# Kernel optimization log

Measured on AMD Instinct MI355X. Metric: run time of the kernel, lower is better.

The kernel has to match this reference:

```python
import jax, jax.numpy as jnp
import numpy as np

EPS_BN = 1e-5
EPS_COS = 1e-8
N, E, D = 50000, 1600000, 128
HGC, LG, NUM_CLASSES, EIN, PAE_H = 64, 4, 2, 12, 128


def setup_inputs() -> dict:
    key = jax.random.key(0)
    ks = jax.random.split(key, 16)
    kaiming = lambda k, fi, fo: jax.random.normal(k, (fi, fo), jnp.float32) * (2.0 / fi) ** 0.5
    glorot = lambda k, shape: jax.random.normal(k, shape, jnp.float32) * (2.0 / (shape[-2] + shape[-1])) ** 0.5
    inp = {}
    inp["features"] = jax.random.normal(ks[0], (N, D), jnp.float32)
    inp["edge_index"] = jax.random.randint(ks[1], (2, E), 0, N, jnp.int32)
    inp["edgenet_input"] = jax.random.normal(ks[2], (E, EIN), jnp.float32)
    # PAE parser: Linear(6,128) -> ReLU -> BN(128) -> Dropout -> Linear(128,128)
    inp["pae_w1"] = kaiming(ks[3], EIN // 2, PAE_H)
    inp["pae_b1"] = jnp.zeros((PAE_H,), jnp.float32)
    inp["pae_bn_g"] = jnp.ones((PAE_H,), jnp.float32)
    inp["pae_bn_b"] = jnp.zeros((PAE_H,), jnp.float32)
    inp["pae_bn_rm"] = jnp.zeros((PAE_H,), jnp.float32)
    inp["pae_bn_rv"] = jnp.ones((PAE_H,), jnp.float32)
    inp["pae_w2"] = kaiming(ks[4], PAE_H, PAE_H)
    inp["pae_b2"] = jnp.zeros((PAE_H,), jnp.float32)
    # ChebConv weights, K=3, bias=False: [K, in, out]
    inp["cheb_w0"] = glorot(ks[5], (3, D, HGC))
    inp["cheb_w1"] = glorot(ks[6], (3, HGC, HGC))
    inp["cheb_w2"] = glorot(ks[7], (3, HGC, HGC))
    inp["cheb_w3"] = glorot(ks[8], (3, HGC, HGC))
    # classifier: Linear(lg*hgc=256, 256) -> ReLU -> BN(256) -> Linear(256, num_classes)
    CLS_IN = LG * HGC
    inp["cls_w1"] = kaiming(ks[9], CLS_IN, 256)
    inp["cls_b1"] = jnp.zeros((256,), jnp.float32)
    inp["cls_bn_g"] = jnp.ones((256,), jnp.float32)
    inp["cls_bn_b"] = jnp.zeros((256,), jnp.float32)
    inp["cls_bn_rm"] = jnp.zeros((256,), jnp.float32)
    inp["cls_bn_rv"] = jnp.ones((256,), jnp.float32)
    inp["cls_w2"] = kaiming(ks[10], 256, NUM_CLASSES)
    inp["cls_b2"] = jnp.zeros((NUM_CLASSES,), jnp.float32)
    return inp


def _bn_eval(h, g, b, rm, rv):
    return (h - rm) * jax.lax.rsqrt(rv + EPS_BN) * g + b


def _pae(x, w1, b1, g, b, rm, rv, w2, b2):
    half = w1.shape[0]
    def enc(z):
        h = jax.nn.relu(z @ w1 + b1)
        h = _bn_eval(h, g, b, rm, rv)
        return h @ w2 + b2                      # [E, PAE_H]
    h1, h2 = enc(x[:, :half]), enc(x[:, half:])
    num = jnp.sum(h1 * h2, axis=1)
    den = jnp.maximum(jnp.linalg.norm(h1, axis=1) * jnp.linalg.norm(h2, axis=1), EPS_COS)
    return (num / den + 1.0) * 0.5              # cosine sim mapped to [0, 1]


def _cheb_conv(x, W, row, col, norm, n_nodes):
    # (the +I from L and the -I self-loops with fill=-1 cancel in the propagation)
    def lhat(z):
        return jax.ops.segment_sum(norm[:, None] * z[col], row, num_segments=n_nodes)
    Tx0 = x
    Tx1 = lhat(Tx0)
    Tx2 = 2.0 * lhat(Tx1) - Tx0
    return Tx0 @ W[0] + Tx1 @ W[1] + Tx2 @ W[2]


def reference(features, edge_index, edgenet_input,
              pae_w1, pae_b1, pae_bn_g, pae_bn_b, pae_bn_rm, pae_bn_rv, pae_w2, pae_b2,
              cheb_w0, cheb_w1, cheb_w2, cheb_w3,
              cls_w1, cls_b1, cls_bn_g, cls_bn_b, cls_bn_rm, cls_bn_rv, cls_w2, cls_b2):
    n_nodes = features.shape[0]
    row, col = edge_index[0], edge_index[1]
    # learned edge weights
    edge_weight = _pae(edgenet_input, pae_w1, pae_b1, pae_bn_g, pae_bn_b,
                       pae_bn_rm, pae_bn_rv, pae_w2, pae_b2)
    # sym-normalized (negative) adjacency weights of the scaled Laplacian
    deg = jax.ops.segment_sum(edge_weight, row, num_segments=n_nodes)
    dis = jnp.where(deg > 0, jax.lax.rsqrt(jnp.where(deg > 0, deg, 1.0)), 0.0)
    norm = -dis[row] * edge_weight * dis[col]
    # GCN stack with jumping-knowledge concat (eval mode: dropout is identity)
    h = jax.nn.relu(_cheb_conv(features, cheb_w0, row, col, norm, n_nodes))
    jk = h
    for W in (cheb_w1, cheb_w2, cheb_w3):
        h = jax.nn.relu(_cheb_conv(h, W, row, col, norm, n_nodes))
        jk = jnp.concatenate((jk, h), axis=1)
    # classifier head
    z = jax.nn.relu(jk @ cls_w1 + cls_b1)
    z = _bn_eval(z, cls_bn_g, cls_bn_b, cls_bn_rm, cls_bn_rv)
    logit = z @ cls_w2 + cls_b2
    return (jk, logit, edge_weight)
```

## Files before the change

kernel.cpp:

```cpp
#include <hip/hip_runtime.h>

#define NN 50000
#define EE 1600000

using u16 = unsigned short;
using u32 = unsigned int;
using u64 = unsigned long long;

typedef float f32x4 __attribute__((ext_vector_type(4)));
typedef __bf16 bf16x8 __attribute__((ext_vector_type(8)));
typedef unsigned short u16x8 __attribute__((ext_vector_type(8)));

struct alignas(8) U16x4 { u16 a, b, c, d; };
struct PtrTab { const void* p[20]; };

#define OW1 0
#define OB1 768
#define OG 896
#define OBB 1024
#define ORM 1152
#define ORV 1280
#define OW2 1408
#define OB2 17792
#define OCH0 17920
#define OCH1 42496
#define OCH2 54784
#define OCH3 67072
#define OCW1 79360
#define OCB1 144896
#define OCG 145152
#define OCBB 145408
#define OCRM 145664
#define OCRV 145920
#define OCW2 146176
#define OCB2 146688
#define OTOT 146690

#define LG_OFF ((size_t)NN * 256)
#define EW_OFF ((size_t)NN * 256 + (size_t)NN * 2)

__device__ __forceinline__ float bf2f(u16 u) { return __builtin_bit_cast(float, (u32)u << 16); }
__device__ __forceinline__ float bfl(u32 u) { return __builtin_bit_cast(float, u << 16); }
__device__ __forceinline__ float bfh(u32 u) { return __builtin_bit_cast(float, u & 0xffff0000u); }
__device__ __forceinline__ u16 f2bf(float f) {
    u32 u = __builtin_bit_cast(u32, f);
    return (u16)((u + 0x7fffu + ((u >> 16) & 1u)) >> 16);
}

__global__ __launch_bounds__(256) void k_detect(const u16* __restrict__ f, int* __restrict__ flag) {
    __shared__ int bad;
    if (threadIdx.x == 0) bad = 0;
    __syncthreads();
    u16 u = f[threadIdx.x];
    int e = (u >> 7) & 0xFF;
    if (e >= 0x90) atomicAdd(&bad, 1);
    __syncthreads();
    if (threadIdx.x == 0) flag[0] = (bad < 16) ? 1 : 0;
}

__global__ __launch_bounds__(256) void k_wconv(PtrTab tab, const int* __restrict__ flag,
                                               float* __restrict__ wpad) {
    const int SZ[20] = {768, 128, 128, 128, 128, 128, 16384, 128, 24576, 12288, 12288, 12288,
                        65536, 256, 256, 256, 256, 256, 512, 2};
    const int OF[20] = {OW1, OB1, OG, OBB, ORM, ORV, OW2, OB2, OCH0, OCH1, OCH2, OCH3,
                        OCW1, OCB1, OCG, OCBB, OCRM, OCRV, OCW2, OCB2};
    int a = blockIdx.x;
    int n = SZ[a];
    float* dst = wpad + OF[a];
    if (flag[0] != 0) {
        const u16* s = (const u16*)tab.p[a];
        for (int i = threadIdx.x; i < n; i += 256) dst[i] = bf2f(s[i]);
    } else {
        const float* s = (const float*)tab.p[a];
        for (int i = threadIdx.x; i < n; i += 256) dst[i] = s[i];
    }
}

__global__ __launch_bounds__(128) void k_fold(const float* __restrict__ wpad,
                                              u16* __restrict__ W2s, float* __restrict__ b2p) {
    const float* g = wpad + OG;
    const float* b = wpad + OBB;
    const float* rm = wpad + ORM;
    const float* rv = wpad + ORV;
    const float* w2 = wpad + OW2;
    const float* b2 = wpad + OB2;
    int blk = blockIdx.x, tid = threadIdx.x;
    if (blk < 32) {
        int kc = blk >> 3, jt = blk & 7;
        int lane = tid & 63, jh = tid >> 6;
        int q = lane >> 4;
        for (int jj = 0; jj < 4; jj++) {
            int j = jh * 4 + jj;
            int k = kc * 32 + ((j < 4) ? (q * 4 + j) : (16 + q * 4 + (j - 4)));
            int jcol = jt * 16 + (lane & 15);
            float s = g[k] * rsqrtf(rv[k] + 1e-5f);
            W2s[((kc * 8 + jt) * 64 + lane) * 8 + j] = f2bf(s * w2[k * 128 + jcol]);
        }
    } else {
        if (tid < 128) {
            int j = tid;
            float acc = b2[j];
            for (int k = 0; k < 128; k++) {
                float s = g[k] * rsqrtf(rv[k] + 1e-5f);
                float t = b[k] - rm[k] * s;
                acc += t * w2[k * 128 + j];
            }
            b2p[j] = acc;
        }
    }
}

__global__ __launch_bounds__(256) void k_foldc(const float* __restrict__ wpad,
                                               u16* __restrict__ W1c, float* __restrict__ w2p,
                                               float* __restrict__ b2p2) {
    int tid = threadIdx.x;
    if (blockIdx.x < 64) {
        const float* w1 = wpad + OCW1;
        int base = blockIdx.x * 1024 + tid * 4;
#pragma unroll
        for (int u = 0; u < 4; u++) {
            int gi = base + u;
            int j = gi & 7;
            int lane = (gi >> 3) & 63;
            int ct = (gi >> 9) & 15;
            int kc2 = (gi >> 13) & 1;
            int l = gi >> 14;
            int k = l * 64 + kc2 * 32 + ((lane >> 4) & 3) * 8 + j;
            int col = ct * 16 + (lane & 15);
            W1c[gi] = f2bf(w1[k * 256 + col]);
        }
    } else {
        __shared__ float red[8];
        int j = tid;
        float s = wpad[OCG + j] * rsqrtf(wpad[OCRV + j] + 1e-5f);
        float t = wpad[OCBB + j] - wpad[OCRM + j] * s;
        float w0 = wpad[OCW2 + j * 2], w1v = wpad[OCW2 + j * 2 + 1];
        w2p[j * 2] = s * w0;
        w2p[j * 2 + 1] = s * w1v;
        float c0 = t * w0, c1 = t * w1v;
#pragma unroll
        for (int off = 1; off < 64; off <<= 1) {
            c0 += __shfl_xor(c0, off);
            c1 += __shfl_xor(c1, off);
        }
        int wv = tid >> 6, lane = tid & 63;
        if (lane == 0) { red[wv * 2] = c0; red[wv * 2 + 1] = c1; }
        __syncthreads();
        if (tid == 0) b2p2[0] = wpad[OCB2] + red[0] + red[2] + red[4] + red[6];
        if (tid == 1) b2p2[1] = wpad[OCB2 + 1] + red[1] + red[3] + red[5] + red[7];
    }
}

__global__ __launch_bounds__(256) void k_foldw(const float* __restrict__ wpad,
                                               u16* __restrict__ Wf0, u16* __restrict__ Wf1,
                                               u16* __restrict__ Wf2, u16* __restrict__ Wf3) {
    int b = blockIdx.x, tid = threadIdx.x;
    const float* src;
    u16* dst;
    int nkt;
    if (b < 24)      { src = wpad + OCH0; dst = Wf0; nkt = 12; }
    else if (b < 36) { src = wpad + OCH1; dst = Wf1; b -= 24; nkt = 6; }
    else if (b < 48) { src = wpad + OCH2; dst = Wf2; b -= 36; nkt = 6; }
    else             { src = wpad + OCH3; dst = Wf3; b -= 48; nkt = 6; }
    int base = b * 1024 + tid * 4;
#pragma unroll
    for (int u = 0; u < 4; u++) {
        int gi = base + u;
        int jj = gi & 7;
        int lane = (gi >> 3) & 63;
        int ct = (gi >> 9) & 3;
        int kt = gi >> 11;
        if (kt < nkt) {
            int k = kt * 32 + ((lane >> 4) & 3) * 8 + jj;
            int col = ct * 16 + (lane & 15);
            dst[gi] = f2bf(src[k * 64 + col]);
        }
    }
}

__global__ __launch_bounds__(256) void k_x0(const void* __restrict__ feat, const int* __restrict__ flag,
                                            u16* __restrict__ X0) {
    int i = blockIdx.x * 256 + threadIdx.x;
    if (flag[0] != 0) {
        ((uint4*)X0)[i] = ((const uint4*)feat)[i];
    } else {
        const float4* f = (const float4*)feat;
        float4 a = f[2 * i], b = f[2 * i + 1];
        u16x8 o;
        o[0] = f2bf(a.x); o[1] = f2bf(a.y); o[2] = f2bf(a.z); o[3] = f2bf(a.w);
        o[4] = f2bf(b.x); o[5] = f2bf(b.y); o[6] = f2bf(b.z); o[7] = f2bf(b.w);
        ((uint4*)X0)[i] = __builtin_bit_cast(uint4, o);
    }
}

__global__ __launch_bounds__(256, 3) void k_pae(const void* __restrict__ zin, const float* __restrict__ wpad,
                                                const u16* __restrict__ W2sg, const float* __restrict__ b2p,
                                                const int* __restrict__ ei, const int* __restrict__ flag,
                                                float* __restrict__ ewf, void* __restrict__ dout,
                                                u64* __restrict__ dc) {
    __shared__ __align__(16) u16 sW2[16384];
    __shared__ float sB2[128];
    int tid = threadIdx.x;
    for (int i = tid; i < 8192; i += 256) ((u32*)sW2)[i] = ((const u32*)W2sg)[i];
    if (tid < 128) sB2[tid] = b2p[tid];
    __syncthreads();

    bool isbf = flag[0] != 0;
    int wv = __builtin_amdgcn_readfirstlane(tid >> 6);
    int lane = tid & 63;
    int quad = lane >> 4, lrow = lane & 15, jc = lane & 15;
    u32 qm = (quad == 0) ? 0xffffffffu : 0u;

    uint4 w1f[8];
    f32x4 cb[8];
#pragma unroll
    for (int kt = 0; kt < 8; kt++) {
        u32 a = 0, b = 0, c = 0;
        if (quad == 0) {
            int col = kt * 16 + lrow;
            a = (u32)f2bf(wpad[OW1 + 0 * 128 + col]) | ((u32)f2bf(wpad[OW1 + 1 * 128 + col]) << 16);
            b = (u32)f2bf(wpad[OW1 + 2 * 128 + col]) | ((u32)f2bf(wpad[OW1 + 3 * 128 + col]) << 16);
            c = (u32)f2bf(wpad[OW1 + 4 * 128 + col]) | ((u32)f2bf(wpad[OW1 + 5 * 128 + col]) << 16);
        }
        w1f[kt] = (uint4){a, b, c, 0u};
#pragma unroll
        for (int r = 0; r < 4; r++) cb[kt][r] = wpad[OB1 + kt * 16 + quad * 4 + r];
    }

    int gw = blockIdx.x * 4 + wv;
    const int ngroups = EE / 16;
    const int gstep = gridDim.x * 4;

    uint2 pb0, pb1, pb2;
    float4 pf0, pf1, pf2;
    if (gw < ngroups) {
        if (isbf) {
            const uint2* zp = (const uint2*)((const u16*)zin + (size_t)(gw * 16 + lrow) * 12);
            pb0 = zp[0]; pb1 = zp[1]; pb2 = zp[2];
        } else {
            const float4* zp = (const float4*)((const float*)zin + (size_t)(gw * 16 + lrow) * 12);
            pf0 = zp[0]; pf1 = zp[1]; pf2 = zp[2];
        }
    }

#pragma unroll 1
    for (int gidx = gw; gidx < ngroups; gidx += gstep) {
        int e0 = gidx * 16;
        float z1[6], z2[6];
        if (isbf) {
            z1[0] = bfl(pb0.x); z1[1] = bfh(pb0.x); z1[2] = bfl(pb0.y); z1[3] = bfh(pb0.y);
            z1[4] = bfl(pb1.x); z1[5] = bfh(pb1.x);
            z2[0] = bfl(pb1.y); z2[1] = bfh(pb1.y); z2[2] = bfl(pb2.x); z2[3] = bfh(pb2.x);
            z2[4] = bfl(pb2.y); z2[5] = bfh(pb2.y);
        } else {
            z1[0] = pf0.x; z1[1] = pf0.y; z1[2] = pf0.z; z1[3] = pf0.w; z1[4] = pf1.x; z1[5] = pf1.y;
            z2[0] = pf1.z; z2[1] = pf1.w; z2[2] = pf2.x; z2[3] = pf2.y; z2[4] = pf2.z; z2[5] = pf2.w;
        }
        int gn = gidx + gstep;
        if (gn < ngroups) {
            if (isbf) {
                const uint2* zp = (const uint2*)((const u16*)zin + (size_t)(gn * 16 + lrow) * 12);
                pb0 = zp[0]; pb1 = zp[1]; pb2 = zp[2];
            } else {
                const float4* zp = (const float4*)((const float*)zin + (size_t)(gn * 16 + lrow) * 12);
                pf0 = zp[0]; pf1 = zp[1]; pf2 = zp[2];
            }
        }
        int rows[4];
        if (jc == 0) {
#pragma unroll
            for (int r = 0; r < 4; r++) rows[r] = ei[e0 + quad * 4 + r];
        }

        u32 za0, za1, za2, zb0, zb1, zb2;
        asm("v_cvt_pk_bf16_f32 %0, %1, %2" : "=v"(za0) : "v"(z1[0]), "v"(z1[1]));
        asm("v_cvt_pk_bf16_f32 %0, %1, %2" : "=v"(za1) : "v"(z1[2]), "v"(z1[3]));
        asm("v_cvt_pk_bf16_f32 %0, %1, %2" : "=v"(za2) : "v"(z1[4]), "v"(z1[5]));
        asm("v_cvt_pk_bf16_f32 %0, %1, %2" : "=v"(zb0) : "v"(z2[0]), "v"(z2[1]));
        asm("v_cvt_pk_bf16_f32 %0, %1, %2" : "=v"(zb1) : "v"(z2[2]), "v"(z2[3]));
        asm("v_cvt_pk_bf16_f32 %0, %1, %2" : "=v"(zb2) : "v"(z2[4]), "v"(z2[5]));
        uint4 zu1 = {za0 & qm, za1 & qm, za2 & qm, 0u};
        uint4 zu2 = {zb0 & qm, zb1 & qm, zb2 & qm, 0u};
        bf16x8 zf1 = __builtin_bit_cast(bf16x8, zu1);
        bf16x8 zf2 = __builtin_bit_cast(bf16x8, zu2);

        bf16x8 a1f[4], a2f[4];
        {
            f32x4 c1[8];
#pragma unroll
            for (int kt = 0; kt < 8; kt++)
                c1[kt] = __builtin_amdgcn_mfma_f32_16x16x32_bf16(
                    __builtin_bit_cast(bf16x8, w1f[kt]), zf1, cb[kt], 0, 0, 0);
#pragma unroll
            for (int kc = 0; kc < 4; kc++) {
                float h0 = fmaxf(c1[2 * kc][0], 0.f), h1 = fmaxf(c1[2 * kc][1], 0.f);
                float h2 = fmaxf(c1[2 * kc][2], 0.f), h3 = fmaxf(c1[2 * kc][3], 0.f);
                float h4 = fmaxf(c1[2 * kc + 1][0], 0.f), h5 = fmaxf(c1[2 * kc + 1][1], 0.f);
                float h6 = fmaxf(c1[2 * kc + 1][2], 0.f), h7 = fmaxf(c1[2 * kc + 1][3], 0.f);
                u32 p0, p1, p2, p3;
                asm("v_cvt_pk_bf16_f32 %0, %1, %2" : "=v"(p0) : "v"(h0), "v"(h1));
                asm("v_cvt_pk_bf16_f32 %0, %1, %2" : "=v"(p1) : "v"(h2), "v"(h3));
                asm("v_cvt_pk_bf16_f32 %0, %1, %2" : "=v"(p2) : "v"(h4), "v"(h5));
                asm("v_cvt_pk_bf16_f32 %0, %1, %2" : "=v"(p3) : "v"(h6), "v"(h7));
                uint4 au = {p0, p1, p2, p3};
                a1f[kc] = __builtin_bit_cast(bf16x8, au);
            }
        }
        {
            f32x4 c2[8];
#pragma unroll
            for (int kt = 0; kt < 8; kt++)
                c2[kt] = __builtin_amdgcn_mfma_f32_16x16x32_bf16(
                    __builtin_bit_cast(bf16x8, w1f[kt]), zf2, cb[kt], 0, 0, 0);
#pragma unroll
            for (int kc = 0; kc < 4; kc++) {
                float h0 = fmaxf(c2[2 * kc][0], 0.f), h1 = fmaxf(c2[2 * kc][1], 0.f);
                float h2 = fmaxf(c2[2 * kc][2], 0.f), h3 = fmaxf(c2[2 * kc][3], 0.f);
                float h4 = fmaxf(c2[2 * kc + 1][0], 0.f), h5 = fmaxf(c2[2 * kc + 1][1], 0.f);
                float h6 = fmaxf(c2[2 * kc + 1][2], 0.f), h7 = fmaxf(c2[2 * kc + 1][3], 0.f);
                u32 p0, p1, p2, p3;
                asm("v_cvt_pk_bf16_f32 %0, %1, %2" : "=v"(p0) : "v"(h0), "v"(h1));
                asm("v_cvt_pk_bf16_f32 %0, %1, %2" : "=v"(p1) : "v"(h2), "v"(h3));
                asm("v_cvt_pk_bf16_f32 %0, %1, %2" : "=v"(p2) : "v"(h4), "v"(h5));
                asm("v_cvt_pk_bf16_f32 %0, %1, %2" : "=v"(p3) : "v"(h6), "v"(h7));
                uint4 au = {p0, p1, p2, p3};
                a2f[kc] = __builtin_bit_cast(bf16x8, au);
            }
        }

        float num[4] = {0, 0, 0, 0}, q1[4] = {0, 0, 0, 0}, q2[4] = {0, 0, 0, 0};
#pragma unroll 1
        for (int jt = 0; jt < 8; jt++) {
            f32x4 acc1 = {0.f, 0.f, 0.f, 0.f}, acc2 = {0.f, 0.f, 0.f, 0.f};
#pragma unroll
            for (int kc = 0; kc < 4; kc++) {
                bf16x8 bb = *reinterpret_cast<const bf16x8*>(&sW2[((kc * 8 + jt) * 64 + lane) * 8]);
                acc1 = __builtin_amdgcn_mfma_f32_16x16x32_bf16(a1f[kc], bb, acc1, 0, 0, 0);
                acc2 = __builtin_amdgcn_mfma_f32_16x16x32_bf16(a2f[kc], bb, acc2, 0, 0, 0);
            }
            float bbias = sB2[jt * 16 + jc];
#pragma unroll
            for (int r = 0; r < 4; r++) {
                float h1 = acc1[r] + bbias;
                float h2 = acc2[r] + bbias;
                num[r] = fmaf(h1, h2, num[r]);
                q1[r] = fmaf(h1, h1, q1[r]);
                q2[r] = fmaf(h2, h2, q2[r]);
            }
        }
#pragma unroll
        for (int off = 1; off < 16; off <<= 1) {
#pragma unroll
            for (int r = 0; r < 4; r++) {
                num[r] += __shfl_xor(num[r], off);
                q1[r] += __shfl_xor(q1[r], off);
                q2[r] += __shfl_xor(q2[r], off);
            }
        }
        if (jc == 0) {
#pragma unroll
            for (int r = 0; r < 4; r++) {
                int e = e0 + quad * 4 + r;
                float den = fmaxf(sqrtf(q1[r]) * sqrtf(q2[r]), 1e-8f);
                float wgt = (num[r] / den + 1.f) * 0.5f;
                if (!(wgt == wgt)) wgt = 0.5f;
                ewf[e] = wgt;
                if (isbf) ((u16*)dout)[EW_OFF + e] = f2bf(wgt);
                else ((float*)dout)[EW_OFF + e] = wgt;
                u32 fx = (u32)(wgt * 8388608.f + 0.5f);
                atomicAdd(dc + rows[r], (((u64)1) << 32) | (u64)fx);
            }
        }
    }
}

__global__ __launch_bounds__(1024) void k_scan(const u64* __restrict__ dc,
                                               int* __restrict__ offs, float* __restrict__ dis) {
    __shared__ int wsum[16];
    __shared__ int carry;
    int tid = threadIdx.x;
    int wv = tid >> 6, lane = tid & 63;
    if (tid == 0) carry = 0;
    __syncthreads();
    for (int c = 0; c < 49; c++) {
        int i = c * 1024 + tid;
        u64 v64 = (i < NN) ? dc[i] : 0ull;
        int v = (int)(v64 >> 32);
        if (i < NN) {
            float d = (float)(u32)v64 * (1.f / 8388608.f);
            dis[i] = d > 0.f ? rsqrtf(d) : 0.f;
        }
        int x = v;
#pragma unroll
        for (int off = 1; off < 64; off <<= 1) {
            int t = __shfl_up(x, off);
            if (lane >= off) x += t;
        }
        if (lane == 63) wsum[wv] = x;
        __syncthreads();
        if (tid < 16) {
            int s = wsum[tid];
#pragma unroll
            for (int off = 1; off < 16; off <<= 1) {
                int t = __shfl_up(s, off, 16);
                if (tid >= off) s += t;
            }
            wsum[tid] = s;
        }
        __syncthreads();
        int base = carry + (wv > 0 ? wsum[wv - 1] : 0);
        if (i < NN) offs[i] = base + x - v;
        __syncthreads();
        if (tid == 0) carry += wsum[15];
        __syncthreads();
    }
    if (tid == 0) offs[NN] = carry;
}

__global__ __launch_bounds__(256) void k_csr(const int* __restrict__ ei, const float* __restrict__ ewf,
                                             const float* __restrict__ dis, const int* __restrict__ offs,
                                             int* __restrict__ cursor, uint2* __restrict__ csr_meta) {
    int e = blockIdx.x * 256 + threadIdx.x;
    int r = ei[e], c = ei[EE + e];
    float wgt = ewf[e];
    int pos = offs[r] + atomicAdd(cursor + r, 1);
    float nrm = -dis[r] * wgt * dis[c];
    csr_meta[pos] = make_uint2((u32)c, __builtin_bit_cast(u32, nrm));
}

template <int F>
__global__ __launch_bounds__(256) void k_prop(const u16* __restrict__ src, const uint2* __restrict__ csr_meta,
                                              const int* __restrict__ offs,
                                              u16* __restrict__ out, const u16* __restrict__ base,
                                              float alpha, float beta) {
    int lane = threadIdx.x & 63;
    int wv = threadIdx.x >> 6;
    int node = blockIdx.x * 4 + wv;
    int s = offs[node], e = offs[node + 1];

    if (F == 128) {
        int sub = lane >> 4;
        int fl = lane & 15;
        const uint4* sv = (const uint4*)src;
        float a[8] = {0, 0, 0, 0, 0, 0, 0, 0};
        int p = s;
        if (p + 7 < e) {
            uint2 m0 = csr_meta[p + sub];
            uint2 m1 = csr_meta[p + 4 + sub];
            while (true) {
                uint4 v0 = sv[(size_t)m0.x * 16 + fl];
                uint4 v1 = sv[(size_t)m1.x * 16 + fl];
                float w0 = __builtin_bit_cast(float, m0.y);
                float w1 = __builtin_bit_cast(float, m1.y);
                p += 8;
                bool more = (p + 7 < e);
                if (more) {
                    m0 = csr_meta[p + sub];
                    m1 = csr_meta[p + 4 + sub];
                }
                a[0] = fmaf(w0, bfl(v0.x), a[0]); a[1] = fmaf(w0, bfh(v0.x), a[1]);
                a[2] = fmaf(w0, bfl(v0.y), a[2]); a[3] = fmaf(w0, bfh(v0.y), a[3]);
                a[4] = fmaf(w0, bfl(v0.z), a[4]); a[5] = fmaf(w0, bfh(v0.z), a[5]);
                a[6] = fmaf(w0, bfl(v0.w), a[6]); a[7] = fmaf(w0, bfh(v0.w), a[7]);
                a[0] = fmaf(w1, bfl(v1.x), a[0]); a[1] = fmaf(w1, bfh(v1.x), a[1]);
                a[2] = fmaf(w1, bfl(v1.y), a[2]); a[3] = fmaf(w1, bfh(v1.y), a[3]);
                a[4] = fmaf(w1, bfl(v1.z), a[4]); a[5] = fmaf(w1, bfh(v1.z), a[5]);
                a[6] = fmaf(w1, bfl(v1.w), a[6]); a[7] = fmaf(w1, bfh(v1.w), a[7]);
                if (!more) break;
            }
        }
        if (p + 3 < e) {
            uint2 m0 = csr_meta[p + sub];
            uint4 v0 = sv[(size_t)m0.x * 16 + fl];
            float w0 = __builtin_bit_cast(float, m0.y);
            a[0] = fmaf(w0, bfl(v0.x), a[0]); a[1] = fmaf(w0, bfh(v0.x), a[1]);
            a[2] = fmaf(w0, bfl(v0.y), a[2]); a[3] = fmaf(w0, bfh(v0.y), a[3]);
            a[4] = fmaf(w0, bfl(v0.z), a[4]); a[5] = fmaf(w0, bfh(v0.z), a[5]);
            a[6] = fmaf(w0, bfl(v0.w), a[6]); a[7] = fmaf(w0, bfh(v0.w), a[7]);
            p += 4;
        }
#pragma unroll
        for (int i = 0; i < 8; i++) {
            a[i] += __shfl_xor(a[i], 16);
            a[i] += __shfl_xor(a[i], 32);
        }
        if (sub == 0) {
            for (; p < e; p++) {
                uint2 m0 = csr_meta[p];
                uint4 v = sv[(size_t)m0.x * 16 + fl];
                float w = __builtin_bit_cast(float, m0.y);
                a[0] = fmaf(w, bfl(v.x), a[0]); a[1] = fmaf(w, bfh(v.x), a[1]);
                a[2] = fmaf(w, bfl(v.y), a[2]); a[3] = fmaf(w, bfh(v.y), a[3]);
                a[4] = fmaf(w, bfl(v.z), a[4]); a[5] = fmaf(w, bfh(v.z), a[5]);
                a[6] = fmaf(w, bfl(v.w), a[6]); a[7] = fmaf(w, bfh(v.w), a[7]);
            }
            float o[8];
#pragma unroll
            for (int i = 0; i < 8; i++) o[i] = alpha * a[i];
            if (beta != 0.f) {
                uint4 bv = ((const uint4*)base)[(size_t)node * 16 + fl];
                o[0] = fmaf(beta, bfl(bv.x), o[0]); o[1] = fmaf(beta, bfh(bv.x), o[1]);
                o[2] = fmaf(beta, bfl(bv.y), o[2]); o[3] = fmaf(beta, bfh(bv.y), o[3]);
                o[4] = fmaf(beta, bfl(bv.z), o[4]); o[5] = fmaf(beta, bfh(bv.z), o[5]);
                o[6] = fmaf(beta, bfl(bv.w), o[6]); o[7] = fmaf(beta, bfh(bv.w), o[7]);
            }
            uint4 ov;
            ov.x = (u32)f2bf(o[0]) | ((u32)f2bf(o[1]) << 16);
            ov.y = (u32)f2bf(o[2]) | ((u32)f2bf(o[3]) << 16);
            ov.z = (u32)f2bf(o[4]) | ((u32)f2bf(o[5]) << 16);
            ov.w = (u32)f2bf(o[6]) | ((u32)f2bf(o[7]) << 16);
            ((uint4*)out)[(size_t)node * 16 + fl] = ov;
        }
    } else {
        int sub = lane >> 3;
        int fl = lane & 7;
        const uint4* sv = (const uint4*)src;
        float a[8] = {0, 0, 0, 0, 0, 0, 0, 0};
        int p = s;
        if (p + 15 < e) {
            uint2 m0 = csr_meta[p + sub];
            uint2 m1 = csr_meta[p + 8 + sub];
            while (true) {
                uint4 v0 = sv[(size_t)m0.x * 8 + fl];
                uint4 v1 = sv[(size_t)m1.x * 8 + fl];
                float w0 = __builtin_bit_cast(float, m0.y);
                float w1 = __builtin_bit_cast(float, m1.y);
                p += 16;
                bool more = (p + 15 < e);
                if (more) {
                    m0 = csr_meta[p + sub];
                    m1 = csr_meta[p + 8 + sub];
                }
                a[0] = fmaf(w0, bfl(v0.x), a[0]); a[1] = fmaf(w0, bfh(v0.x), a[1]);
                a[2] = fmaf(w0, bfl(v0.y), a[2]); a[3] = fmaf(w0, bfh(v0.y), a[3]);
                a[4] = fmaf(w0, bfl(v0.z), a[4]); a[5] = fmaf(w0, bfh(v0.z), a[5]);
                a[6] = fmaf(w0, bfl(v0.w), a[6]); a[7] = fmaf(w0, bfh(v0.w), a[7]);
                a[0] = fmaf(w1, bfl(v1.x), a[0]); a[1] = fmaf(w1, bfh(v1.x), a[1]);
                a[2] = fmaf(w1, bfl(v1.y), a[2]); a[3] = fmaf(w1, bfh(v1.y), a[3]);
                a[4] = fmaf(w1, bfl(v1.z), a[4]); a[5] = fmaf(w1, bfh(v1.z), a[5]);
                a[6] = fmaf(w1, bfl(v1.w), a[6]); a[7] = fmaf(w1, bfh(v1.w), a[7]);
                if (!more) break;
            }
        }
        if (p + 7 < e) {
            uint2 m0 = csr_meta[p + sub];
            uint4 v0 = sv[(size_t)m0.x * 8 + fl];
            float w0 = __builtin_bit_cast(float, m0.y);
            a[0] = fmaf(w0, bfl(v0.x), a[0]); a[1] = fmaf(w0, bfh(v0.x), a[1]);
            a[2] = fmaf(w0, bfl(v0.y), a[2]); a[3] = fmaf(w0, bfh(v0.y), a[3]);
            a[4] = fmaf(w0, bfl(v0.z), a[4]); a[5] = fmaf(w0, bfh(v0.z), a[5]);
            a[6] = fmaf(w0, bfl(v0.w), a[6]); a[7] = fmaf(w0, bfh(v0.w), a[7]);
            p += 8;
        }
#pragma unroll
        for (int i = 0; i < 8; i++) {
            a[i] += __shfl_xor(a[i], 8);
            a[i] += __shfl_xor(a[i], 16);
            a[i] += __shfl_xor(a[i], 32);
        }
        if (sub == 0) {
            for (; p < e; p++) {
                uint2 m0 = csr_meta[p];
                uint4 v = sv[(size_t)m0.x * 8 + fl];
                float w = __builtin_bit_cast(float, m0.y);
                a[0] = fmaf(w, bfl(v.x), a[0]); a[1] = fmaf(w, bfh(v.x), a[1]);
                a[2] = fmaf(w, bfl(v.y), a[2]); a[3] = fmaf(w, bfh(v.y), a[3]);
                a[4] = fmaf(w, bfl(v.z), a[4]); a[5] = fmaf(w, bfh(v.z), a[5]);
                a[6] = fmaf(w, bfl(v.w), a[6]); a[7] = fmaf(w, bfh(v.w), a[7]);
            }
            float o[8];
#pragma unroll
            for (int i = 0; i < 8; i++) o[i] = alpha * a[i];
            if (beta != 0.f) {
                uint4 bv = ((const uint4*)base)[(size_t)node * 8 + fl];
                o[0] = fmaf(beta, bfl(bv.x), o[0]); o[1] = fmaf(beta, bfh(bv.x), o[1]);
                o[2] = fmaf(beta, bfl(bv.y), o[2]); o[3] = fmaf(beta, bfh(bv.y), o[3]);
                o[4] = fmaf(beta, bfl(bv.z), o[4]); o[5] = fmaf(beta, bfh(bv.z), o[5]);
                o[6] = fmaf(beta, bfl(bv.w), o[6]); o[7] = fmaf(beta, bfh(bv.w), o[7]);
            }
            uint4 ov;
            ov.x = (u32)f2bf(o[0]) | ((u32)f2bf(o[1]) << 16);
            ov.y = (u32)f2bf(o[2]) | ((u32)f2bf(o[3]) << 16);
            ov.z = (u32)f2bf(o[4]) | ((u32)f2bf(o[5]) << 16);
            ov.w = (u32)f2bf(o[6]) | ((u32)f2bf(o[7]) << 16);
            ((uint4*)out)[(size_t)node * 8 + fl] = ov;
        }
    }
}

template <int F>
__global__ __launch_bounds__(256) void k_gemm(const u16* __restrict__ X0, const u16* __restrict__ X1,
                                              const u16* __restrict__ X2, const u16* __restrict__ Wf,
                                              u16* __restrict__ Hout, void* __restrict__ jk, int jkoff,
                                              const int* __restrict__ flag) {
    constexpr int KT = (3 * F) / 32;
    __shared__ __align__(16) u16 sB[KT * 4 * 64 * 8];
    int tid = threadIdx.x;
    for (int i = tid; i < KT * 4 * 64 * 4; i += 256) ((u32*)sB)[i] = ((const u32*)Wf)[i];
    __syncthreads();

    bool isbf = flag[0] != 0;
    int wv = __builtin_amdgcn_readfirstlane(tid >> 6);
    int lane = tid & 63;
    int quad = lane >> 4, jc = lane & 15;
    int pair = wv >> 1;
    int half = wv & 1;
    int nb = blockIdx.x * 32 + pair * 16;
    int row = nb + jc;
    if (row > NN - 1) row = NN - 1;

    uint4 av[KT];
#pragma unroll
    for (int kt = 0; kt < KT; kt++) {
        int kg = kt * 32 + quad * 8;
        const u16* Xp;
        int kk;
        if (kg < F) { Xp = X0; kk = kg; }
        else if (kg < 2 * F) { Xp = X1; kk = kg - F; }
        else { Xp = X2; kk = kg - 2 * F; }
        av[kt] = *(const uint4*)(Xp + (size_t)row * F + kk);
    }

    f32x4 acc0 = {0.f, 0.f, 0.f, 0.f}, acc1 = {0.f, 0.f, 0.f, 0.f};
#pragma unroll
    for (int kt = 0; kt < KT; kt++) {
        bf16x8 af = __builtin_bit_cast(bf16x8, av[kt]);
        bf16x8 b0 = *reinterpret_cast<const bf16x8*>(&sB[((kt * 4 + half * 2 + 0) * 64 + lane) * 8]);
        bf16x8 b1 = *reinterpret_cast<const bf16x8*>(&sB[((kt * 4 + half * 2 + 1) * 64 + lane) * 8]);
        acc0 = __builtin_amdgcn_mfma_f32_16x16x32_bf16(af, b0, acc0, 0, 0, 0);
        acc1 = __builtin_amdgcn_mfma_f32_16x16x32_bf16(af, b1, acc1, 0, 0, 0);
    }

#pragma unroll
    for (int ct = 0; ct < 2; ct++) {
        f32x4 a = ct ? acc1 : acc0;
        int j = (half * 2 + ct) * 16 + jc;
#pragma unroll
        for (int r = 0; r < 4; r++) {
            int n = nb + quad * 4 + r;
            if (n < NN) {
                float v = fmaxf(a[r], 0.f);
                Hout[(size_t)n * 64 + j] = f2bf(v);
                if (isbf) ((u16*)jk)[(size_t)n * 256 + jkoff + j] = f2bf(v);
                else ((float*)jk)[(size_t)n * 256 + jkoff + j] = v;
            }
        }
    }
}

__global__ __launch_bounds__(256) void k_cls(const u16* __restrict__ h0, const u16* __restrict__ h1,
                                             const u16* __restrict__ h2, const u16* __restrict__ h3,
                                             const u16* __restrict__ W1c, const float* __restrict__ wpad,
                                             const float* __restrict__ w2p, const float* __restrict__ b2p2,
                                             const int* __restrict__ flag, void* __restrict__ dout) {
    __shared__ __align__(16) u16 sB[16384];
    __shared__ float sb1[256];
    __shared__ float sw2[512];
    __shared__ float sb2[2];
    __shared__ float part[4][16][2];
    int tid = threadIdx.x;
    if (tid < 256) sb1[tid] = wpad[OCB1 + tid];
    for (int i = tid; i < 512; i += 256) sw2[i] = w2p[i];
    if (tid < 2) sb2[tid] = b2p2[tid];

    int wv = __builtin_amdgcn_readfirstlane(tid >> 6);
    int lane = tid & 63;
    int quad = lane >> 4, jc = lane & 15;
    int pair = wv >> 1;
    int half = wv & 1;
    int nb = blockIdx.x * 32 + pair * 16;

    f32x4 acc[8] = {{0.f, 0.f, 0.f, 0.f}, {0.f, 0.f, 0.f, 0.f}, {0.f, 0.f, 0.f, 0.f}, {0.f, 0.f, 0.f, 0.f},
                    {0.f, 0.f, 0.f, 0.f}, {0.f, 0.f, 0.f, 0.f}, {0.f, 0.f, 0.f, 0.f}, {0.f, 0.f, 0.f, 0.f}};
    const u16* hs[4] = {h0, h1, h2, h3};

    int row = nb + jc;
    if (row > NN - 1) row = NN - 1;

#pragma unroll 1
    for (int l = 0; l < 4; l++) {
        __syncthreads();
        const u32* src = (const u32*)W1c + l * 8192;
        for (int i = tid; i < 8192; i += 256) ((u32*)sB)[i] = src[i];
        __syncthreads();
        const uint4* rp = (const uint4*)(hs[l] + (size_t)row * 64);
        uint4 a0u = rp[quad], a1u = rp[4 + quad];
        bf16x8 af0 = __builtin_bit_cast(bf16x8, a0u);
        bf16x8 af1 = __builtin_bit_cast(bf16x8, a1u);
#pragma unroll
        for (int jt = 0; jt < 8; jt++) {
            int ct = half * 8 + jt;
            bf16x8 b0 = *reinterpret_cast<const bf16x8*>(&sB[((0 * 16 + ct) * 64 + lane) * 8]);
            bf16x8 b1f = *reinterpret_cast<const bf16x8*>(&sB[((1 * 16 + ct) * 64 + lane) * 8]);
            acc[jt] = __builtin_amdgcn_mfma_f32_16x16x32_bf16(af0, b0, acc[jt], 0, 0, 0);
            acc[jt] = __builtin_amdgcn_mfma_f32_16x16x32_bf16(af1, b1f, acc[jt], 0, 0, 0);
        }
    }

    float p0[4] = {0, 0, 0, 0}, p1[4] = {0, 0, 0, 0};
#pragma unroll
    for (int jt = 0; jt < 8; jt++) {
        int j = (half * 8 + jt) * 16 + jc;
        float b1v = sb1[j], wa = sw2[2 * j], wb = sw2[2 * j + 1];
#pragma unroll
        for (int r = 0; r < 4; r++) {
            float h = fmaxf(acc[jt][r] + b1v, 0.f);
            p0[r] = fmaf(h, wa, p0[r]);
            p1[r] = fmaf(h, wb, p1[r]);
        }
    }
#pragma unroll
    for (int off = 1; off < 16; off <<= 1) {
#pragma unroll
        for (int r = 0; r < 4; r++) {
            p0[r] += __shfl_xor(p0[r], off);
            p1[r] += __shfl_xor(p1[r], off);
        }
    }
    if (jc == 0) {
#pragma unroll
        for (int r = 0; r < 4; r++) {
            part[wv][quad * 4 + r][0] = p0[r];
            part[wv][quad * 4 + r][1] = p1[r];
        }
    }
    __syncthreads();
    if (tid < 32) {
        int rl = tid & 15, p = tid >> 4;
        int n = blockIdx.x * 32 + tid;
        if (n < NN) {
            float l0 = part[2 * p][rl][0] + part[2 * p + 1][rl][0] + sb2[0];
            float l1 = part[2 * p][rl][1] + part[2 * p + 1][rl][1] + sb2[1];
            if (flag[0] != 0) {
                u32 pack = (u32)f2bf(l0) | ((u32)f2bf(l1) << 16);
                *(u32*)((u16*)dout + LG_OFF + (size_t)n * 2) = pack;
            } else {
                float2 o = {l0, l1};
                *(float2*)((float*)dout + LG_OFF + (size_t)n * 2) = o;
            }
        }
    }
}

extern "C" void kernel_launch(void* const* d_in, const int* in_sizes, int n_in,
                              void* d_out, int out_size, void* d_ws, size_t ws_size,
                              hipStream_t stream) {
    const void* features = d_in[0];
    const int* ei = (const int*)d_in[1];
    const void* zin = d_in[2];

    char* w = (char*)d_ws;
    auto alloc = [&](size_t bytes) -> void* {
        void* p = (void*)w;
        w += (bytes + 255) & ~(size_t)255;
        return p;
    };
    u16* X0 = (u16*)alloc((size_t)NN * 128 * 2);
    u16* Tx1 = (u16*)alloc((size_t)NN * 128 * 2);
    u16* Tx2 = (u16*)alloc((size_t)NN * 128 * 2);
    u16* h0 = (u16*)alloc((size_t)NN * 64 * 2);
    u16* h1 = (u16*)alloc((size_t)NN * 64 * 2);
    u16* h2 = (u16*)alloc((size_t)NN * 64 * 2);
    u16* h3 = (u16*)alloc((size_t)NN * 64 * 2);
    float* ewf = (float*)alloc((size_t)EE * 4);
    uint2* csr_meta = (uint2*)alloc((size_t)EE * 8);
    u64* dc = (u64*)alloc((size_t)NN * 8);
    int* cursor = (int*)alloc((size_t)NN * 4);
    float* dis = (float*)alloc((size_t)NN * 4);
    int* offs = (int*)alloc((size_t)(NN + 1) * 4);
    u16* W2s = (u16*)alloc((size_t)16384 * 2);
    float* b2p = (float*)alloc((size_t)128 * 4);
    u16* W1c = (u16*)alloc((size_t)65536 * 2);
    float* w2p = (float*)alloc((size_t)512 * 4);
    float* b2p2 = (float*)alloc((size_t)2 * 4);
    u16* Wf0 = (u16*)alloc((size_t)24576 * 2);
    u16* Wf1 = (u16*)alloc((size_t)12288 * 2);
    u16* Wf2 = (u16*)alloc((size_t)12288 * 2);
    u16* Wf3 = (u16*)alloc((size_t)12288 * 2);
    float* wpad = (float*)alloc((size_t)OTOT * 4);
    int* flag = (int*)alloc(256);

    hipMemsetAsync(dc, 0, (size_t)((char*)dis - (char*)dc), stream);

    PtrTab tab;
    for (int i = 0; i < 20; i++) tab.p[i] = d_in[3 + i];

    k_detect<<<1, 256, 0, stream>>>((const u16*)features, flag);
    k_wconv<<<20, 256, 0, stream>>>(tab, flag, wpad);
    k_fold<<<33, 128, 0, stream>>>(wpad, W2s, b2p);
    k_foldc<<<65, 256, 0, stream>>>(wpad, W1c, w2p, b2p2);
    k_foldw<<<60, 256, 0, stream>>>(wpad, Wf0, Wf1, Wf2, Wf3);
    k_x0<<<3125, 256, 0, stream>>>(features, flag, X0);
    k_pae<<<768, 256, 0, stream>>>(zin, wpad, W2s, b2p, ei, flag, ewf, d_out, dc);
    k_scan<<<1, 1024, 0, stream>>>(dc, offs, dis);
    k_csr<<<EE / 256, 256, 0, stream>>>(ei, ewf, dis, offs, cursor, csr_meta);

    k_prop<128><<<12500, 256, 0, stream>>>(X0, csr_meta, offs, Tx1, nullptr, 1.f, 0.f);
    k_prop<128><<<12500, 256, 0, stream>>>(Tx1, csr_meta, offs, Tx2, X0, 2.f, -1.f);
    k_gemm<128><<<1563, 256, 0, stream>>>(X0, Tx1, Tx2, Wf0, h0, d_out, 0, flag);
    k_prop<64><<<12500, 256, 0, stream>>>(h0, csr_meta, offs, Tx1, nullptr, 1.f, 0.f);
    k_prop<64><<<12500, 256, 0, stream>>>(Tx1, csr_meta, offs, Tx2, h0, 2.f, -1.f);
    k_gemm<64><<<1563, 256, 0, stream>>>(h0, Tx1, Tx2, Wf1, h1, d_out, 64, flag);
    k_prop<64><<<12500, 256, 0, stream>>>(h1, csr_meta, offs, Tx1, nullptr, 1.f, 0.f);
    k_prop<64><<<12500, 256, 0, stream>>>(Tx1, csr_meta, offs, Tx2, h1, 2.f, -1.f);
    k_gemm<64><<<1563, 256, 0, stream>>>(h1, Tx1, Tx2, Wf2, h2, d_out, 128, flag);
    k_prop<64><<<12500, 256, 0, stream>>>(h2, csr_meta, offs, Tx1, nullptr, 1.f, 0.f);
    k_prop<64><<<12500, 256, 0, stream>>>(Tx1, csr_meta, offs, Tx2, h2, 2.f, -1.f);
    k_gemm<64><<<1563, 256, 0, stream>>>(h2, Tx1, Tx2, Wf3, h3, d_out, 192, flag);

    k_cls<<<1563, 256, 0, stream>>>(h0, h1, h2, h3, W1c, wpad, w2p, b2p2, flag, d_out);
    (void)in_sizes; (void)n_in; (void)out_size; (void)ws_size;
}
```

Baseline: 978.5 us.

## Project first Chebyshev layer before propagation to shrink gathered features

The first ChebConv layer is rewritten algebraically. X0 is multiplied once by stacked weights to give [X0·W1 | X0·W2] (128 columns) and X0·(W0−W2) (64 columns). Propagation then runs on the projected features, and the second hop gathers only 64 of the 128 columns, fused with the final add, ReLU and jk write. This replaces two 128-wide gathers plus a 384-K GEMM with one 128-wide and one 64-wide gather. A separate change packs the PAE cosine accumulation into v_pk_add/v_pk_fma instructions. The cost is that projection happens before propagation, which changes bf16 rounding order.

New measurement: 979.9 us. No clear change (+0.1%).

```diff
diff --git a/kernel.cpp b/kernel.cpp
--- a/kernel.cpp
+++ b/kernel.cpp
@@ -8,6 +8,7 @@
 using u64 = unsigned long long;
 
 typedef float f32x4 __attribute__((ext_vector_type(4)));
+typedef float f32x2 __attribute__((ext_vector_type(2)));
 typedef __bf16 bf16x8 __attribute__((ext_vector_type(8)));
 typedef unsigned short u16x8 __attribute__((ext_vector_type(8)));
 
@@ -152,16 +153,14 @@
 }
 
 __global__ __launch_bounds__(256) void k_foldw(const float* __restrict__ wpad,
-                                               u16* __restrict__ Wf0, u16* __restrict__ Wf1,
+                                               u16* __restrict__ Wf1,
                                                u16* __restrict__ Wf2, u16* __restrict__ Wf3) {
     int b = blockIdx.x, tid = threadIdx.x;
     const float* src;
     u16* dst;
-    int nkt;
-    if (b < 24)      { src = wpad + OCH0; dst = Wf0; nkt = 12; }
-    else if (b < 36) { src = wpad + OCH1; dst = Wf1; b -= 24; nkt = 6; }
-    else if (b < 48) { src = wpad + OCH2; dst = Wf2; b -= 36; nkt = 6; }
-    else             { src = wpad + OCH3; dst = Wf3; b -= 48; nkt = 6; }
+    if (b < 12)      { src = wpad + OCH1; dst = Wf1; }
+    else if (b < 24) { src = wpad + OCH2; dst = Wf2; b -= 12; }
+    else             { src = wpad + OCH3; dst = Wf3; b -= 24; }
     int base = b * 1024 + tid * 4;
 #pragma unroll
     for (int u = 0; u < 4; u++) {
@@ -170,11 +169,37 @@
         int lane = (gi >> 3) & 63;
         int ct = (gi >> 9) & 3;
         int kt = gi >> 11;
-        if (kt < nkt) {
-            int k = kt * 32 + ((lane >> 4) & 3) * 8 + jj;
-            int col = ct * 16 + (lane & 15);
-            dst[gi] = f2bf(src[k * 64 + col]);
-        }
+        int k = kt * 32 + ((lane >> 4) & 3) * 8 + jj;
+        int col = ct * 16 + (lane & 15);
+        dst[gi] = f2bf(src[k * 64 + col]);
+    }
+}
+
+__global__ __launch_bounds__(256) void k_foldw0(const float* __restrict__ wpad,
+                                                u16* __restrict__ Wg0) {
+    const float* src = wpad + OCH0;
+    int tid = threadIdx.x;
+    int base = blockIdx.x * 1024 + tid * 4;
+#pragma unroll
+    for (int u = 0; u < 4; u++) {
+        int gi = base + u;
+        int jj = gi & 7;
+        int lane = (gi >> 3) & 63;
+        int rest = gi >> 9;
+        int ct = rest % 12;
+        int kt = rest / 12;
+        int k = kt * 32 + ((lane >> 4) & 3) * 8 + jj;
+        int cl = (lane & 15);
+        float v;
+        if (ct < 4) {
+            v = src[(1 * 128 + k) * 64 + ct * 16 + cl];
+        } else if (ct < 8) {
+            v = src[(2 * 128 + k) * 64 + (ct - 4) * 16 + cl];
+        } else {
+            int c = (ct - 8) * 16 + cl;
+            v = src[(0 * 128 + k) * 64 + c] - src[(2 * 128 + k) * 64 + c];
+        }
+        Wg0[gi] = f2bf(v);
     }
 }
 
@@ -328,7 +353,9 @@
             }
         }
 
-        float num[4] = {0, 0, 0, 0}, q1[4] = {0, 0, 0, 0}, q2[4] = {0, 0, 0, 0};
+        f32x2 numA = {0.f, 0.f}, numB = {0.f, 0.f};
+        f32x2 q1A = {0.f, 0.f}, q1B = {0.f, 0.f};
+        f32x2 q2A = {0.f, 0.f}, q2B = {0.f, 0.f};
 #pragma unroll 1
         for (int jt = 0; jt < 8; jt++) {
             f32x4 acc1 = {0.f, 0.f, 0.f, 0.f}, acc2 = {0.f, 0.f, 0.f, 0.f};
@@ -339,15 +366,24 @@
                 acc2 = __builtin_amdgcn_mfma_f32_16x16x32_bf16(a2f[kc], bb, acc2, 0, 0, 0);
             }
             float bbias = sB2[jt * 16 + jc];
-#pragma unroll
-            for (int r = 0; r < 4; r++) {
-                float h1 = acc1[r] + bbias;
-                float h2 = acc2[r] + bbias;
-                num[r] = fmaf(h1, h2, num[r]);
-                q1[r] = fmaf(h1, h1, q1[r]);
-                q2[r] = fmaf(h2, h2, q2[r]);
-            }
-        }
+            f32x2 bb2 = {bbias, bbias};
+            f32x2 a1lo = {acc1[0], acc1[1]}, a1hi = {acc1[2], acc1[3]};
+            f32x2 a2lo = {acc2[0], acc2[1]}, a2hi = {acc2[2], acc2[3]};
+            f32x2 h1A, h1B, h2A, h2B;
+            asm("v_pk_add_f32 %0, %1, %2" : "=v"(h1A) : "v"(a1lo), "v"(bb2));
+            asm("v_pk_add_f32 %0, %1, %2" : "=v"(h1B) : "v"(a1hi), "v"(bb2));
+            asm("v_pk_add_f32 %0, %1, %2" : "=v"(h2A) : "v"(a2lo), "v"(bb2));
+            asm("v_pk_add_f32 %0, %1, %2" : "=v"(h2B) : "v"(a2hi), "v"(bb2));
+            asm("v_pk_fma_f32 %0, %1, %2, %0" : "+v"(numA) : "v"(h1A), "v"(h2A));
+            asm("v_pk_fma_f32 %0, %1, %2, %0" : "+v"(numB) : "v"(h1B), "v"(h2B));
+            asm("v_pk_fma_f32 %0, %1, %2, %0" : "+v"(q1A) : "v"(h1A), "v"(h1A));
+            asm("v_pk_fma_f32 %0, %1, %2, %0" : "+v"(q1B) : "v"(h1B), "v"(h1B));
+            asm("v_pk_fma_f32 %0, %1, %2, %0" : "+v"(q2A) : "v"(h2A), "v"(h2A));
+            asm("v_pk_fma_f32 %0, %1, %2, %0" : "+v"(q2B) : "v"(h2B), "v"(h2B));
+        }
+        float num[4] = {numA[0], numA[1], numB[0], numB[1]};
+        float q1[4] = {q1A[0], q1A[1], q1B[0], q1B[1]};
+        float q2[4] = {q2A[0], q2A[1], q2B[0], q2B[1]};
 #pragma unroll
         for (int off = 1; off < 16; off <<= 1) {
 #pragma unroll
@@ -588,6 +624,145 @@
     }
 }
 
+__global__ __launch_bounds__(256) void k_prop0b(const u16* __restrict__ V, const uint2* __restrict__ csr_meta,
+                                                const int* __restrict__ offs, const u16* __restrict__ D,
+                                                u16* __restrict__ h0out, const int* __restrict__ flag,
+                                                void* __restrict__ jkout) {
+    int lane = threadIdx.x & 63;
+    int wv = threadIdx.x >> 6;
+    int node = blockIdx.x * 4 + wv;
+    int s = offs[node], e = offs[node + 1];
+    int sub = lane >> 3;
+    int fl = lane & 7;
+    const uint4* sv = (const uint4*)V;
+    float a[8] = {0, 0, 0, 0, 0, 0, 0, 0};
+    int p = s;
+    if (p + 15 < e) {
+        uint2 m0 = csr_meta[p + sub];
+        uint2 m1 = csr_meta[p + 8 + sub];
+        while (true) {
+            uint4 v0 = sv[(size_t)m0.x * 16 + 8 + fl];
+            uint4 v1 = sv[(size_t)m1.x * 16 + 8 + fl];
+            float w0 = __builtin_bit_cast(float, m0.y);
+            float w1 = __builtin_bit_cast(float, m1.y);
+            p += 16;
+            bool more = (p + 15 < e);
+            if (more) {
+                m0 = csr_meta[p + sub];
+                m1 = csr_meta[p + 8 + sub];
+            }
+            a[0] = fmaf(w0, bfl(v0.x), a[0]); a[1] = fmaf(w0, bfh(v0.x), a[1]);
+            a[2] = fmaf(w0, bfl(v0.y), a[2]); a[3] = fmaf(w0, bfh(v0.y), a[3]);
+            a[4] = fmaf(w0, bfl(v0.z), a[4]); a[5] = fmaf(w0, bfh(v0.z), a[5]);
+            a[6] = fmaf(w0, bfl(v0.w), a[6]); a[7] = fmaf(w0, bfh(v0.w), a[7]);
+            a[0] = fmaf(w1, bfl(v1.x), a[0]); a[1] = fmaf(w1, bfh(v1.x), a[1]);
+            a[2] = fmaf(w1, bfl(v1.y), a[2]); a[3] = fmaf(w1, bfh(v1.y), a[3]);
+            a[4] = fmaf(w1, bfl(v1.z), a[4]); a[5] = fmaf(w1, bfh(v1.z), a[5]);
+            a[6] = fmaf(w1, bfl(v1.w), a[6]); a[7] = fmaf(w1, bfh(v1.w), a[7]);
+            if (!more) break;
+        }
+    }
+    if (p + 7 < e) {
+        uint2 m0 = csr_meta[p + sub];
+        uint4 v0 = sv[(size_t)m0.x * 16 + 8 + fl];
+        float w0 = __builtin_bit_cast(float, m0.y);
+        a[0] = fmaf(w0, bfl(v0.x), a[0]); a[1] = fmaf(w0, bfh(v0.x), a[1]);
+        a[2] = fmaf(w0, bfl(v0.y), a[2]); a[3] = fmaf(w0, bfh(v0.y), a[3]);
+        a[4] = fmaf(w0, bfl(v0.z), a[4]); a[5] = fmaf(w0, bfh(v0.z), a[5]);
+        a[6] = fmaf(w0, bfl(v0.w), a[6]); a[7] = fmaf(w0, bfh(v0.w), a[7]);
+        p += 8;
+    }
+#pragma unroll
+    for (int i = 0; i < 8; i++) {
+        a[i] += __shfl_xor(a[i], 8);
+        a[i] += __shfl_xor(a[i], 16);
+        a[i] += __shfl_xor(a[i], 32);
+    }
+    if (sub == 0) {
+        for (; p < e; p++) {
+            uint2 m0 = csr_meta[p];
+            uint4 v = sv[(size_t)m0.x * 16 + 8 + fl];
+            float w = __builtin_bit_cast(float, m0.y);
+            a[0] = fmaf(w, bfl(v.x), a[0]); a[1] = fmaf(w, bfh(v.x), a[1]);
+            a[2] = fmaf(w, bfl(v.y), a[2]); a[3] = fmaf(w, bfh(v.y), a[3]);
+            a[4] = fmaf(w, bfl(v.z), a[4]); a[5] = fmaf(w, bfh(v.z), a[5]);
+            a[6] = fmaf(w, bfl(v.w), a[6]); a[7] = fmaf(w, bfh(v.w), a[7]);
+        }
+        uint4 v1 = sv[(size_t)node * 16 + fl];
+        uint4 dv = ((const uint4*)D)[(size_t)node * 8 + fl];
+        float o[8];
+        o[0] = fmaf(2.f, a[0], bfl(v1.x) + bfl(dv.x)); o[1] = fmaf(2.f, a[1], bfh(v1.x) + bfh(dv.x));
+        o[2] = fmaf(2.f, a[2], bfl(v1.y) + bfl(dv.y)); o[3] = fmaf(2.f, a[3], bfh(v1.y) + bfh(dv.y));
+        o[4] = fmaf(2.f, a[4], bfl(v1.z) + bfl(dv.z)); o[5] = fmaf(2.f, a[5], bfh(v1.z) + bfh(dv.z));
+        o[6] = fmaf(2.f, a[6], bfl(v1.w) + bfl(dv.w)); o[7] = fmaf(2.f, a[7], bfh(v1.w) + bfh(dv.w));
+#pragma unroll
+        for (int i = 0; i < 8; i++) o[i] = fmaxf(o[i], 0.f);
+        uint4 ov;
+        ov.x = (u32)f2bf(o[0]) | ((u32)f2bf(o[1]) << 16);
+        ov.y = (u32)f2bf(o[2]) | ((u32)f2bf(o[3]) << 16);
+        ov.z = (u32)f2bf(o[4]) | ((u32)f2bf(o[5]) << 16);
+        ov.w = (u32)f2bf(o[6]) | ((u32)f2bf(o[7]) << 16);
+        ((uint4*)h0out)[(size_t)node * 8 + fl] = ov;
+        if (flag[0] != 0) {
+            ((uint4*)jkout)[(size_t)node * 32 + fl] = ov;
+        } else {
+            float* jf = (float*)jkout + (size_t)node * 256 + fl * 8;
+#pragma unroll
+            for (int i = 0; i < 8; i++) jf[i] = o[i];
+        }
+    }
+}
+
+__global__ __launch_bounds__(256) void k_gemm0(const u16* __restrict__ X0, const u16* __restrict__ Wg0,
+                                               u16* __restrict__ U, u16* __restrict__ D) {
+    __shared__ __align__(16) u16 sB[4 * 12 * 64 * 8];
+    int tid = threadIdx.x;
+    for (int i = tid; i < 12288; i += 256) ((u32*)sB)[i] = ((const u32*)Wg0)[i];
+    __syncthreads();
+
+    int wv = __builtin_amdgcn_readfirstlane(tid >> 6);
+    int lane = tid & 63;
+    int quad = lane >> 4, jc = lane & 15;
+    int pair = wv >> 1;
+    int half = wv & 1;
+    int nb = blockIdx.x * 32 + pair * 16;
+    int row = nb + jc;
+    if (row > NN - 1) row = NN - 1;
+
+    uint4 av[4];
+#pragma unroll
+    for (int kt = 0; kt < 4; kt++)
+        av[kt] = *(const uint4*)(X0 + (size_t)row * 128 + kt * 32 + quad * 8);
+
+    f32x4 acc[6] = {{0.f, 0.f, 0.f, 0.f}, {0.f, 0.f, 0.f, 0.f}, {0.f, 0.f, 0.f, 0.f},
+                    {0.f, 0.f, 0.f, 0.f}, {0.f, 0.f, 0.f, 0.f}, {0.f, 0.f, 0.f, 0.f}};
+#pragma unroll
+    for (int kt = 0; kt < 4; kt++) {
+        bf16x8 af = __builtin_bit_cast(bf16x8, av[kt]);
+#pragma unroll
+        for (int ct = 0; ct < 6; ct++) {
+            int g = half * 6 + ct;
+            bf16x8 b0 = *reinterpret_cast<const bf16x8*>(&sB[((kt * 12 + g) * 64 + lane) * 8]);
+            acc[ct] = __builtin_amdgcn_mfma_f32_16x16x32_bf16(af, b0, acc[ct], 0, 0, 0);
+        }
+    }
+
+#pragma unroll
+    for (int ct = 0; ct < 6; ct++) {
+        int g = half * 6 + ct;
+        int j = g * 16 + jc;
+#pragma unroll
+        for (int r = 0; r < 4; r++) {
+            int n = nb + quad * 4 + r;
+            if (n < NN) {
+                float v = acc[ct][r];
+                if (j < 128) U[(size_t)n * 128 + j] = f2bf(v);
+                else D[(size_t)n * 64 + (j - 128)] = f2bf(v);
+            }
+        }
+    }
+}
+
 template <int F>
 __global__ __launch_bounds__(256) void k_gemm(const u16* __restrict__ X0, const u16* __restrict__ X1,
                                               const u16* __restrict__ X2, const u16* __restrict__ Wf,
@@ -762,6 +937,7 @@
     u16* h1 = (u16*)alloc((size_t)NN * 64 * 2);
     u16* h2 = (u16*)alloc((size_t)NN * 64 * 2);
     u16* h3 = (u16*)alloc((size_t)NN * 64 * 2);
+    u16* Dbuf = (u16*)alloc((size_t)NN * 64 * 2);
     float* ewf = (float*)alloc((size_t)EE * 4);
     uint2* csr_meta = (uint2*)alloc((size_t)EE * 8);
     u64* dc = (u64*)alloc((size_t)NN * 8);
@@ -773,7 +949,7 @@
     u16* W1c = (u16*)alloc((size_t)65536 * 2);
     float* w2p = (float*)alloc((size_t)512 * 4);
     float* b2p2 = (float*)alloc((size_t)2 * 4);
-    u16* Wf0 = (u16*)alloc((size_t)24576 * 2);
+    u16* Wg0 = (u16*)alloc((size_t)24576 * 2);
     u16* Wf1 = (u16*)alloc((size_t)12288 * 2);
     u16* Wf2 = (u16*)alloc((size_t)12288 * 2);
     u16* Wf3 = (u16*)alloc((size_t)12288 * 2);
@@ -789,15 +965,16 @@
     k_wconv<<<20, 256, 0, stream>>>(tab, flag, wpad);
     k_fold<<<33, 128, 0, stream>>>(wpad, W2s, b2p);
     k_foldc<<<65, 256, 0, stream>>>(wpad, W1c, w2p, b2p2);
-    k_foldw<<<60, 256, 0, stream>>>(wpad, Wf0, Wf1, Wf2, Wf3);
+    k_foldw0<<<24, 256, 0, stream>>>(wpad, Wg0);
+    k_foldw<<<36, 256, 0, stream>>>(wpad, Wf1, Wf2, Wf3);
     k_x0<<<3125, 256, 0, stream>>>(features, flag, X0);
     k_pae<<<768, 256, 0, stream>>>(zin, wpad, W2s, b2p, ei, flag, ewf, d_out, dc);
     k_scan<<<1, 1024, 0, stream>>>(dc, offs, dis);
     k_csr<<<EE / 256, 256, 0, stream>>>(ei, ewf, dis, offs, cursor, csr_meta);
 
-    k_prop<128><<<12500, 256, 0, stream>>>(X0, csr_meta, offs, Tx1, nullptr, 1.f, 0.f);
-    k_prop<128><<<12500, 256, 0, stream>>>(Tx1, csr_meta, offs, Tx2, X0, 2.f, -1.f);
-    k_gemm<128><<<1563, 256, 0, stream>>>(X0, Tx1, Tx2, Wf0, h0, d_out, 0, flag);
+    k_gemm0<<<1563, 256, 0, stream>>>(X0, Wg0, Tx1 , Dbuf);
+    k_prop<128><<<12500, 256, 0, stream>>>(Tx1, csr_meta, offs, Tx2 , nullptr, 1.f, 0.f);
+    k_prop0b<<<12500, 256, 0, stream>>>(Tx2, csr_meta, offs, Dbuf, h0, flag, d_out);
     k_prop<64><<<12500, 256, 0, stream>>>(h0, csr_meta, offs, Tx1, nullptr, 1.f, 0.f);
     k_prop<64><<<12500, 256, 0, stream>>>(Tx1, csr_meta, offs, Tx2, h0, 2.f, -1.f);
     k_gemm<64><<<1563, 256, 0, stream>>>(h0, Tx1, Tx2, Wf1, h1, d_out, 64, flag);
```
